# Kernel optimization log

Hardware: AMD Instinct MI355X
Metric: run time of the kernel (lower is better)

Reference implementation:

```python
import jax, jax.numpy as jnp
import numpy as np

M = 4096
N = 4096


def precompute_expk(n):
    # Twiddle factors exp(-i*pi*k/(2n)), k = 0..n-1 (matches DREAMPlace precompute_expk)
    k = jnp.arange(n)
    return jnp.exp(-1j * jnp.pi * k.astype(jnp.float32) / (2.0 * n)).astype(jnp.complex64)


def setup_inputs() -> dict:
    key = jax.random.key(0)
    x = jax.random.normal(key, (M, N), dtype=jnp.float32)
    return {"x": x, "expkM": precompute_expk(M), "expkN": precompute_expk(N)}


def _dct1d(x, expk):
    """DCT-II along the last axis via Makhoul's even/odd reorder + FFT + twiddle.

    y[k] = sum_n x[n] * cos(pi * (2n+1) * k / (2L))  (unnormalized, no factor 2)
    """
    # reorder: even-indexed samples forward, odd-indexed samples reversed
    v = jnp.concatenate([x[..., 0::2], x[..., 1::2][..., ::-1]], axis=-1)
    V = jnp.fft.fft(v, axis=-1)
    return jnp.real(V * expk)


def reference(x, expkM, expkN):
    # 2D DCT-II: transform columns (length N), then rows (length M)
    y = _dct1d(x, expkN)            # [M, N], DCT along axis -1
    y = _dct1d(y.T, expkM).T        # DCT along axis 0
    return y
```

## Files before the change

### kernel.cpp

```cpp
#include <hip/hip_runtime.h>
#include <hip/hip_bf16.h>


#define L 4096

__device__ __forceinline__ float2 cmul(float2 a, float2 b) {
    return make_float2(a.x * b.x - a.y * b.y, a.x * b.y + a.y * b.x);
}

__device__ __forceinline__ void bfly4(float2& x0, float2& x1, float2& x2, float2& x3) {
    float t0x = x0.x + x2.x, t0y = x0.y + x2.y;
    float t1x = x0.x - x2.x, t1y = x0.y - x2.y;
    float t2x = x1.x + x3.x, t2y = x1.y + x3.y;
    float t3x = x1.x - x3.x, t3y = x1.y - x3.y;
    x0 = make_float2(t0x + t2x, t0y + t2y);
    x1 = make_float2(t1x + t3y, t1y - t3x);
    x2 = make_float2(t0x - t2x, t0y - t2y);
    x3 = make_float2(t1x - t3y, t1y + t3x);
}

#define FOR8(X) X(0) X(1) X(2) X(3) X(4) X(5) X(6) X(7)

#define FFT8N(P) \
  bfly4(P##0, P##2, P##4, P##6); \
  bfly4(P##1, P##3, P##5, P##7); \
  { float2 e1_=P##2, e2_=P##4, e3_=P##6, o0_=P##1, o1_=P##3, o2_=P##5, o3_=P##7; \
    o1_ = cmul(o1_, make_float2(0.70710678118654752f, -0.70710678118654752f)); \
    o2_ = make_float2(o2_.y, -o2_.x); \
    o3_ = cmul(o3_, make_float2(-0.70710678118654752f, -0.70710678118654752f)); \
    float2 e0_=P##0; \
    P##0 = make_float2(e0_.x+o0_.x, e0_.y+o0_.y); \
    P##4 = make_float2(e0_.x-o0_.x, e0_.y-o0_.y); \
    P##1 = make_float2(e1_.x+o1_.x, e1_.y+o1_.y); \
    P##5 = make_float2(e1_.x-o1_.x, e1_.y-o1_.y); \
    P##2 = make_float2(e2_.x+o2_.x, e2_.y+o2_.y); \
    P##6 = make_float2(e2_.x-o2_.x, e2_.y-o2_.y); \
    P##3 = make_float2(e3_.x+o3_.x, e3_.y+o3_.y); \
    P##7 = make_float2(e3_.x-o3_.x, e3_.y-o3_.y); }

#define TWCHAIN(P, W) { float2 f_ = W; \
    P##1 = cmul(P##1, f_); f_ = cmul(f_, W); \
    P##2 = cmul(P##2, f_); f_ = cmul(f_, W); \
    P##3 = cmul(P##3, f_); f_ = cmul(f_, W); \
    P##4 = cmul(P##4, f_); f_ = cmul(f_, W); \
    P##5 = cmul(P##5, f_); f_ = cmul(f_, W); \
    P##6 = cmul(P##6, f_); f_ = cmul(f_, W); \
    P##7 = cmul(P##7, f_); }

__global__ __launch_bounds__(512)
void dct_rows4_kernel(const float* __restrict__ in, float* __restrict__ out) {
    __shared__ float2 xch[4160];
    const int l = threadIdx.x & 63;
    const int v = threadIdx.x >> 6;
    const int r0 = blockIdx.x * 2;
    const float* rowA = in + (size_t)r0 * L;
    const float* rowB = rowA + L;

#define LD(u) float2 g##u; { \
        const int n = 512*u + 64*v + l; \
        const int ix = (u < 4) ? (2*n) : (8191 - 2*n); \
        g##u = make_float2(rowA[ix], rowB[ix]); }
    FOR8(LD)
#undef LD

    FFT8N(g)
#define W2(t) xch[512*v + 64*t + l] = g##t;
    FOR8(W2)
#undef W2
    __syncthreads();
#define R2(vv) g##vv = xch[512*vv + 64*v + l];
    FOR8(R2)
#undef R2
    __syncthreads();

    float2 wv; __sincosf((float)v * -0.09817477042468103f, &wv.y, &wv.x);
    TWCHAIN(g, wv)
    FFT8N(g)

    float2 mw, ms;
    __sincosf((float)(l * v) * -1.5339807878856412e-3f, &mw.y, &mw.x);
    __sincosf((float)l * -1.2271846303085130e-2f, &ms.y, &ms.x);
#define W3(s) { g##s = cmul(g##s, mw); xch[520*s + 65*v + l] = g##s; mw = cmul(mw, ms); }
    FOR8(W3)
#undef W3
    __syncthreads();
#define R3(u) g##u = xch[65*l + 8*u + v];
    FOR8(R3)
#undef R3
    __syncthreads();

    FFT8N(g)
#define W4(t) xch[512*v + 64*t + l] = g##t;
    FOR8(W4)
#undef W4
    __syncthreads();
#define R4(vv) g##vv = xch[512*vv + 64*v + l];
    FOR8(R4)
#undef R4
    __syncthreads();

    TWCHAIN(g, wv)
    FFT8N(g)

#define W5(s) xch[520*s + 65*v + l] = g##s;
    FOR8(W5)
#undef W5
    __syncthreads();

    float* outA = out + (size_t)r0 * L;
    float* outB = outA + L;
    float2 e; __sincosf((float)(64*v + l) * 3.8349519697141029e-4f, &e.y, &e.x);
    const float2 ST = make_float2(0.98078528040323045f, 0.19509032201612827f);
#define EP5(s) { \
        const int k = 512*s + 64*v + l; \
        const int m = (4096 - k) & 4095; \
        float2 Zk = g##s; \
        float2 Zm = xch[(m >> 6) * 65 + (m & 63)]; \
        float vax = 0.5f*(Zk.x + Zm.x), vay = 0.5f*(Zk.y - Zm.y); \
        float vbx = 0.5f*(Zk.y + Zm.y), vby = 0.5f*(Zm.x - Zk.x); \
        outA[k] = vax*e.x + vay*e.y; \
        outB[k] = vbx*e.x + vby*e.y; \
        e = cmul(e, ST); }
    FOR8(EP5)
#undef EP5
}

__global__ __launch_bounds__(512)
void fft64_col_a2(const float* __restrict__ Y, float* __restrict__ ws) {
    __shared__ float2 xch[4096];
    const int c = threadIdx.x & 63;
    const int v = threadIdx.x >> 6;
    const int b = blockIdx.x;
    const int T = blockIdx.y;
    const int ca = T * 128 + c;
    const int cb = ca + 64;

#define LDA(u) float2 g##u; { \
        const int aa = 8 * u + v; \
        const int row = (u < 4) ? (128 * aa + 2 * b) : (8191 - 128 * aa - 2 * b); \
        const float* rp = Y + (size_t)row * L; \
        g##u = make_float2(rp[ca], rp[cb]); }
    FOR8(LDA)
#undef LDA

    FFT8N(g)

#define WRA(t) xch[v * 512 + t * 64 + c] = g##t;
    FOR8(WRA)
#undef WRA
    __syncthreads();
#define RDA(vv) g##vv = xch[vv * 512 + v * 64 + c];
    FOR8(RDA)
#undef RDA

    float2 wv; __sincosf((float)v * -0.09817477042468103f, &wv.y, &wv.x);
    TWCHAIN(g, wv)

    FFT8N(g)

    float2 mw, ms;
    __sincosf((float)(b * v) * -1.5339807878856412e-3f, &mw.y, &mw.x);
    __sincosf((float)b * -1.2271846303085130e-2f, &ms.y, &ms.x);
    float2* wp = reinterpret_cast<float2*>(ws) + (size_t)b * 2048 + (size_t)T * 64 + c;
#define STA(s) { \
        g##s = cmul(g##s, mw); \
        wp[(size_t)(8 * s + v) * 131072] = g##s; \
        mw = cmul(mw, ms); }
    FOR8(STA)
#undef STA
}

__global__ __launch_bounds__(512)
void fft64_col_b3(const float* __restrict__ wsf, float* __restrict__ out) {
    __shared__ float2 xch[8192];
    const int c  = threadIdx.x & 63;
    const int v  = threadIdx.x >> 6;
    const int qa = blockIdx.x;
    const int T  = blockIdx.y;
    const int q  = qa;
    const int q2 = (qa == 0) ? 32 : 64 - qa;

    const float2* wsc = reinterpret_cast<const float2*>(wsf);
    const size_t cbase = (size_t)T * 64 + c;

#define LDH(u) \
    float2 ha##u = wsc[(size_t)q  * 131072 + (size_t)(8*u+v) * 2048 + cbase]; \
    float2 hp##u = wsc[(size_t)q2 * 131072 + (size_t)(8*u+v) * 2048 + cbase];
    FOR8(LDH)
#undef LDH

    float2 wv; __sincosf((float)v * -0.09817477042468103f, &wv.y, &wv.x);

    FFT8N(ha)
#define W1(k) xch[v * 512 + k * 64 + c] = ha##k;
    FOR8(W1)
#undef W1
    __syncthreads();
#define DECLG(i) float2 g##i;
    FOR8(DECLG)
#undef DECLG
#define R1b(vv) g##vv = xch[vv * 512 + v * 64 + c];
    FOR8(R1b)
#undef R1b
    TWCHAIN(g, wv)
    FFT8N(g)

#define SV(a) float2 gq##a = g##a; xch[4096 + (8*a + v) * 64 + c] = g##a;
    FOR8(SV)
#undef SV
    __syncthreads();

    FFT8N(hp)
#define W2b(k) xch[v * 512 + k * 64 + c] = hp##k;
    FOR8(W2b)
#undef W2b
    __syncthreads();
#define R2b(vv) g##vv = xch[vv * 512 + v * 64 + c];
    FOR8(R2b)
#undef R2b
    TWCHAIN(g, wv)
    FFT8N(g)
    __syncthreads();
#define W3b(a) xch[(8*a + v) * 64 + c] = g##a;
    FOR8(W3b)
#undef W3b
    __syncthreads();

    const float2 STEP = make_float2(0.98078528040323045f, 0.19509032201612827f);
    float2 eq, eq2;
    __sincosf((float)(64 * v + q ) * 3.8349519697141029e-4f, &eq.y,  &eq.x);
    __sincosf((float)(64 * v + q2) * 3.8349519697141029e-4f, &eq2.y, &eq2.x);
    const int colA = T * 128 + c;

#define CMB(a) { \
    const int p_ = 8 * a + v; \
    float2 rq  = (qa == 0) ? xch[4096 + (((64 - p_) & 63) * 64) + c] \
                           : xch[(63 - p_) * 64 + c]; \
    float2 rq2 = (qa == 0) ? xch[(63 - p_) * 64 + c] \
                           : xch[4096 + (63 - p_) * 64 + c]; \
    float FAx = 0.5f * (gq##a.x + rq.x), FAy = 0.5f * (gq##a.y - rq.y); \
    float FBx = 0.5f * (gq##a.y + rq.y), FBy = 0.5f * (rq.x - gq##a.x); \
    size_t rowq = (size_t)(512 * a + 64 * v + q) * L; \
    out[rowq + colA]      = FAx * eq.x + FAy * eq.y; \
    out[rowq + colA + 64] = FBx * eq.x + FBy * eq.y; \
    float GAx = 0.5f * (g##a.x + rq2.x), GAy = 0.5f * (g##a.y - rq2.y); \
    float GBx = 0.5f * (g##a.y + rq2.y), GBy = 0.5f * (rq2.x - g##a.x); \
    size_t rowq2 = (size_t)(512 * a + 64 * v + q2) * L; \
    out[rowq2 + colA]      = GAx * eq2.x + GAy * eq2.y; \
    out[rowq2 + colA + 64] = GBx * eq2.x + GBy * eq2.y; \
    eq = cmul(eq, STEP); eq2 = cmul(eq2, STEP); }
    FOR8(CMB)
#undef CMB
}

extern "C" void kernel_launch(void* const* d_in, const int* in_sizes, int n_in,
                              void* d_out, int out_size, void* d_ws, size_t ws_size,
                              hipStream_t stream) {
    const float* x = (const float*)d_in[0];
    float* out = (float*)d_out;
    float* ws  = (float*)d_ws;

    dct_rows4_kernel<<<L / 2, 512, 0, stream>>>(x, out);
    fft64_col_a2<<<dim3(64, 32), 512, 0, stream>>>(out, ws);
    fft64_col_b3<<<dim3(32, 32), 512, 0, stream>>>(ws, out);
}
```

Baseline: 73.42 us.

## Split paired column FFTs across two thread halves in 1024-thread blocks

```diff
diff --git a/kernel.cpp b/kernel.cpp
--- a/kernel.cpp
+++ b/kernel.cpp
@@ -170,85 +170,59 @@
 #undef STA
 }
 
-__global__ __launch_bounds__(512)
-void fft64_col_b3(const float* __restrict__ wsf, float* __restrict__ out) {
+__global__ __launch_bounds__(1024)
+void fft64_col_b4(const float* __restrict__ wsf, float* __restrict__ out) {
     __shared__ float2 xch[8192];
     const int c  = threadIdx.x & 63;
-    const int v  = threadIdx.x >> 6;
+    const int v  = (threadIdx.x >> 6) & 7;
+    const int h  = threadIdx.x >> 9;
     const int qa = blockIdx.x;
     const int T  = blockIdx.y;
-    const int q  = qa;
-    const int q2 = (qa == 0) ? 32 : 64 - qa;
+    const int q  = (h == 0) ? qa : ((qa == 0) ? 32 : 64 - qa);
+    const bool self0 = (qa == 0);
+    const int pane = h * 4096;
+    const int ppane = (self0 ? h : 1 - h) * 4096;
 
     const float2* wsc = reinterpret_cast<const float2*>(wsf);
     const size_t cbase = (size_t)T * 64 + c;
 
-#define LDH(u) \
-    float2 ha##u = wsc[(size_t)q  * 131072 + (size_t)(8*u+v) * 2048 + cbase]; \
-    float2 hp##u = wsc[(size_t)q2 * 131072 + (size_t)(8*u+v) * 2048 + cbase];
+#define LDH(u) float2 g##u = wsc[(size_t)q * 131072 + (size_t)(8*u+v) * 2048 + cbase];
     FOR8(LDH)
 #undef LDH
 
     float2 wv; __sincosf((float)v * -0.09817477042468103f, &wv.y, &wv.x);
 
-    FFT8N(ha)
-#define W1(k) xch[v * 512 + k * 64 + c] = ha##k;
+    FFT8N(g)
+#define W1(k) xch[pane + v * 512 + k * 64 + c] = g##k;
     FOR8(W1)
 #undef W1
     __syncthreads();
-#define DECLG(i) float2 g##i;
-    FOR8(DECLG)
-#undef DECLG
-#define R1b(vv) g##vv = xch[vv * 512 + v * 64 + c];
+#define R1b(vv) g##vv = xch[pane + vv * 512 + v * 64 + c];
     FOR8(R1b)
 #undef R1b
-    TWCHAIN(g, wv)
-    FFT8N(g)
-
-#define SV(a) float2 gq##a = g##a; xch[4096 + (8*a + v) * 64 + c] = g##a;
-    FOR8(SV)
-#undef SV
-    __syncthreads();
-
-    FFT8N(hp)
-#define W2b(k) xch[v * 512 + k * 64 + c] = hp##k;
-    FOR8(W2b)
-#undef W2b
-    __syncthreads();
-#define R2b(vv) g##vv = xch[vv * 512 + v * 64 + c];
-    FOR8(R2b)
-#undef R2b
-    TWCHAIN(g, wv)
-    FFT8N(g)
-    __syncthreads();
-#define W3b(a) xch[(8*a + v) * 64 + c] = g##a;
-    FOR8(W3b)
-#undef W3b
+    __syncthreads();
+    TWCHAIN(g, wv)
+    FFT8N(g)
+
+#define WG(a) xch[pane + (8*a + v) * 64 + c] = g##a;
+    FOR8(WG)
+#undef WG
     __syncthreads();
 
     const float2 STEP = make_float2(0.98078528040323045f, 0.19509032201612827f);
-    float2 eq, eq2;
-    __sincosf((float)(64 * v + q ) * 3.8349519697141029e-4f, &eq.y,  &eq.x);
-    __sincosf((float)(64 * v + q2) * 3.8349519697141029e-4f, &eq2.y, &eq2.x);
+    float2 e; __sincosf((float)(64 * v + q) * 3.8349519697141029e-4f, &e.y, &e.x);
     const int colA = T * 128 + c;
 
 #define CMB(a) { \
     const int p_ = 8 * a + v; \
-    float2 rq  = (qa == 0) ? xch[4096 + (((64 - p_) & 63) * 64) + c] \
-                           : xch[(63 - p_) * 64 + c]; \
-    float2 rq2 = (qa == 0) ? xch[(63 - p_) * 64 + c] \
-                           : xch[4096 + (63 - p_) * 64 + c]; \
-    float FAx = 0.5f * (gq##a.x + rq.x), FAy = 0.5f * (gq##a.y - rq.y); \
-    float FBx = 0.5f * (gq##a.y + rq.y), FBy = 0.5f * (rq.x - gq##a.x); \
+    const int pi_ = (q == 0) ? ((64 - p_) & 63) : (63 - p_); \
+    float2 rq = xch[ppane + pi_ * 64 + c]; \
+    float FAx = 0.5f * (g##a.x + rq.x), FAy = 0.5f * (g##a.y - rq.y); \
+    float FBx = 0.5f * (g##a.y + rq.y), FBy = 0.5f * (rq.x - g##a.x); \
     size_t rowq = (size_t)(512 * a + 64 * v + q) * L; \
-    out[rowq + colA]      = FAx * eq.x + FAy * eq.y; \
-    out[rowq + colA + 64] = FBx * eq.x + FBy * eq.y; \
-    float GAx = 0.5f * (g##a.x + rq2.x), GAy = 0.5f * (g##a.y - rq2.y); \
-    float GBx = 0.5f * (g##a.y + rq2.y), GBy = 0.5f * (rq2.x - g##a.x); \
-    size_t rowq2 = (size_t)(512 * a + 64 * v + q2) * L; \
-    out[rowq2 + colA]      = GAx * eq2.x + GAy * eq2.y; \
-    out[rowq2 + colA + 64] = GBx * eq2.x + GBy * eq2.y; \
-    eq = cmul(eq, STEP); eq2 = cmul(eq2, STEP); }
+    out[rowq + colA]      = FAx * e.x + FAy * e.y; \
+    out[rowq + colA + 64] = FBx * e.x + FBy * e.y; \
+    e = cmul(e, STEP); }
     FOR8(CMB)
 #undef CMB
 }
@@ -262,5 +236,5 @@
 
     dct_rows4_kernel<<<L / 2, 512, 0, stream>>>(x, out);
     fft64_col_a2<<<dim3(64, 32), 512, 0, stream>>>(out, ws);
-    fft64_col_b3<<<dim3(32, 32), 512, 0, stream>>>(ws, out);
-}
+    fft64_col_b4<<<dim3(32, 32), 1024, 0, stream>>>(ws, out);
+}
```

New measurement: 73.72 us. Within noise of the previous version (+0.4%).
